# Optimization experiments

Measured on AMD Instinct MI355X. Metric: run time of the kernel, lower is better.

The kernel has to match this reference:

```python
import jax, jax.numpy as jnp
import numpy as np

N_NODES = 65536
N_GRAPHS = 1024
NODES_PER_G = 64
N_EDGES = 1048576
IN_FEATS = 512
HIDDEN = 1024
H4 = 256
EMB = 512
EPS = 1e-5
SLOPE = 0.01


def setup_inputs() -> dict:
    key = jax.random.key(0)
    ks = jax.random.split(key, 10)
    # within-graph random edges: edge e belongs to graph e // (E/B)
    epg = N_EDGES // N_GRAPHS
    eg = np.arange(N_EDGES) // epg
    rng = np.random.default_rng(0)
    src = rng.integers(0, NODES_PER_G, N_EDGES) + eg * NODES_PER_G
    dst = rng.integers(0, NODES_PER_G, N_EDGES) + eg * NODES_PER_G
    node_gid = np.arange(N_NODES) // NODES_PER_G
    return {
        "node_feats": jax.random.normal(ks[0], (N_NODES, IN_FEATS), jnp.float32),
        "edge_weights": jax.random.uniform(ks[1], (N_EDGES,), jnp.float32),
        "W1": jax.random.normal(ks[2], (IN_FEATS, HIDDEN), jnp.float32) * 0.05,
        "W2": jax.random.normal(ks[3], (HIDDEN, H4), jnp.float32) * 0.05,
        "W_emb": jax.random.normal(ks[4], (IN_FEATS + HIDDEN + H4, EMB), jnp.float32) * 0.02,
        "gn1_alpha": jnp.ones((HIDDEN,), jnp.float32),
        "gn1_gamma": jnp.ones((HIDDEN,), jnp.float32),
        "gn1_beta": jnp.zeros((HIDDEN,), jnp.float32),
        "gn2_alpha": jnp.ones((H4,), jnp.float32),
        "gn2_gamma": jnp.ones((H4,), jnp.float32),
        "gn2_beta": jnp.zeros((H4,), jnp.float32),
        "edge_src": jnp.asarray(src, jnp.int32),
        "edge_dst": jnp.asarray(dst, jnp.int32),
        "node_gid": jnp.asarray(node_gid, jnp.int32),
    }


def _seg_sum(x, ids, num):
    return jax.ops.segment_sum(x, ids, num_segments=num)


def _graph_conv(x, W, src, dst, ew):
    # DGL GraphConv, norm='both', bias=False, with edge_weight (u_mul_e)
    ones = jnp.ones((src.shape[0],), x.dtype)
    deg_out = jnp.clip(_seg_sum(ones, src, N_NODES), 1.0)
    deg_in = jnp.clip(_seg_sum(ones, dst, N_NODES), 1.0)
    h = (x * jax.lax.rsqrt(deg_out)[:, None]) @ W
    msg = h[src] * ew[:, None]
    agg = _seg_sum(msg, dst, N_NODES)
    return agg * jax.lax.rsqrt(deg_in)[:, None]


def _graph_norm(x, gid, counts, alpha, gamma, beta):
    # GraphNorm (Cai et al.): learnable mean-scale alpha, per-graph stats
    mean = _seg_sum(x, gid, N_GRAPHS) / counts[:, None]
    sub = x - alpha * mean[gid]
    var = _seg_sum(sub * sub, gid, N_GRAPHS) / counts[:, None]
    return gamma * sub * jax.lax.rsqrt(var[gid] + EPS) + beta


def _mean_nodes(x, gid, counts):
    return _seg_sum(x, gid, N_GRAPHS) / counts[:, None]


def _leaky(x):
    return jnp.where(x >= 0, x, SLOPE * x)


def reference(node_feats, edge_weights, W1, W2, W_emb,
              gn1_alpha, gn1_gamma, gn1_beta,
              gn2_alpha, gn2_gamma, gn2_beta,
              edge_src, edge_dst, node_gid):
    counts = jnp.clip(_seg_sum(jnp.ones((N_NODES,), node_feats.dtype), node_gid, N_GRAPHS), 1.0)
    r0 = _mean_nodes(node_feats, node_gid, counts)                 # [B, in]
    h1 = _graph_conv(node_feats, W1, edge_src, edge_dst, edge_weights)
    h1 = _leaky(_graph_norm(h1, node_gid, counts, gn1_alpha, gn1_gamma, gn1_beta))
    r1 = _mean_nodes(h1, node_gid, counts)                          # [B, hidden]
    h2 = _graph_conv(h1, W2, edge_src, edge_dst, edge_weights)
    h2 = _leaky(_graph_norm(h2, node_gid, counts, gn2_alpha, gn2_gamma, gn2_beta))
    r2 = _mean_nodes(h2, node_gid, counts)                          # [B, hidden/4]
    emb = jnp.concatenate([r0, r1, r2], axis=1) @ W_emb             # [B, EMB]
    # InstanceNorm1d on [B, E] input: per-row normalization, no affine
    mu = jnp.mean(emb, axis=1, keepdims=True)
    var = jnp.mean((emb - mu) ** 2, axis=1, keepdims=True)
    emb = (emb - mu) * jax.lax.rsqrt(var + EPS)
    return _leaky(emb)
```

## Files before the change

### kernel.cpp

```cpp
#include <hip/hip_runtime.h>
#include <hip/hip_bf16.h>
#include <stdint.h>

#define N_NODES   65536
#define N_GRAPHS  1024
#define N_EDGES   1048576
#define IN_FEATS  512
#define HIDDEN    1024
#define H4        256
#define EMB_DIM   512
#define RDIM      1792
#define EPS_F     1e-5f
#define SLOPE_F   0.01f

typedef __bf16 bf16;
typedef __bf16 bf16x8 __attribute__((ext_vector_type(8)));
typedef float  floatx4 __attribute__((ext_vector_type(4)));

#define GLDS16(gp, lp) __builtin_amdgcn_global_load_lds( \
    (const __attribute__((address_space(1))) void*)(gp), \
    (__attribute__((address_space(3))) void*)(lp), 16, 0, 0)

__global__ __launch_bounds__(256) void k_graph_build(
    const int* __restrict__ src, const int* __restrict__ dst,
    const float* __restrict__ ew,
    bf16* __restrict__ adjb, float* __restrict__ scl_o)
{
    __shared__ float sAdj[4096];
    __shared__ float sDegO[64], sDegI[64];
    int g = blockIdx.x, tid = threadIdx.x;
    for (int i = tid; i < 4096; i += 256) sAdj[i] = 0.f;
    if (tid < 64) { sDegO[tid] = 0.f; sDegI[tid] = 0.f; }
    __syncthreads();
    int e0 = g * 1024;
    #pragma unroll
    for (int i = 0; i < 4; ++i) {
        int e = e0 + i * 256 + tid;
        int s = src[e] & 63, d = dst[e] & 63;
        atomicAdd(&sAdj[(d << 6) | s], ew[e]);
        atomicAdd(&sDegO[s], 1.f);
        atomicAdd(&sDegI[d], 1.f);
    }
    __syncthreads();
    if (tid < 64) scl_o[g * 64 + tid] = rsqrtf(fmaxf(sDegO[tid], 1.f));
    bf16* ag = adjb + ((size_t)g << 12);
    for (int i = tid; i < 4096; i += 256) {
        float si = rsqrtf(fmaxf(sDegI[i >> 6], 1.f));
        ag[i] = (bf16)(sAdj[i] * si);
    }
}

__global__ __launch_bounds__(256) void k_transpose(
    const float* __restrict__ W, bf16* __restrict__ WT, int K, int logN)
{
    int idx = blockIdx.x * 256 + threadIdx.x;
    if (idx >= (K << logN)) return;
    int n = idx & ((1 << logN) - 1);
    int k = idx >> logN;
    WT[(size_t)n * K + k] = (bf16)W[idx];
}

__global__ __launch_bounds__(256) void k_prep_agg1(
    const float* __restrict__ x, const float* __restrict__ so,
    const bf16* __restrict__ adjb,
    bf16* __restrict__ axs1, bf16* __restrict__ Rb)
{
    __shared__ __align__(16) bf16 sOut[64 * 264];
    __shared__ float sSo[64];
    int g = blockIdx.x >> 1, half = blockIdx.x & 1;
    int tid = threadIdx.x, lane = tid & 63, wave = tid >> 6, q = lane >> 4;
    if (tid < 64) sSo[tid] = so[g * 64 + tid];
    const float* xg = x + (size_t)g * 64 * IN_FEATS + half * 256;
    const bf16* ag = adjb + ((size_t)g << 12);

    bf16x8 af[4][2];
    #pragma unroll
    for (int mt = 0; mt < 4; ++mt)
        #pragma unroll
        for (int kk = 0; kk < 2; ++kk)
            af[mt][kk] = *(const bf16x8*)&ag[(mt * 16 + (lane & 15)) * 64 + kk * 32 + q * 8];
    __syncthreads();
    float sov[2][8];
    #pragma unroll
    for (int kk = 0; kk < 2; ++kk)
        #pragma unroll
        for (int j = 0; j < 8; ++j) sov[kk][j] = sSo[kk * 32 + q * 8 + j];

    #pragma unroll
    for (int nt = 0; nt < 4; ++nt) {
        int cl = wave * 64 + nt * 16 + (lane & 15);
        floatx4 acc[4] = {};
        float r0 = 0.f;
        #pragma unroll
        for (int kk = 0; kk < 2; ++kk) {
            bf16x8 bfrag;
            #pragma unroll
            for (int j = 0; j < 8; ++j) {
                float v = xg[(size_t)(kk * 32 + q * 8 + j) * IN_FEATS + cl];
                r0 += v;
                bfrag[j] = (bf16)(v * sov[kk][j]);
            }
            #pragma unroll
            for (int mt = 0; mt < 4; ++mt)
                acc[mt] = __builtin_amdgcn_mfma_f32_16x16x32_bf16(af[mt][kk], bfrag, acc[mt], 0, 0, 0);
        }
        r0 += __shfl_xor(r0, 16);
        r0 += __shfl_xor(r0, 32);
        if (lane < 16) Rb[(size_t)g * RDIM + half * 256 + cl] = (bf16)(r0 * (1.f / 64.f));
        #pragma unroll
        for (int mt = 0; mt < 4; ++mt)
            #pragma unroll
            for (int i = 0; i < 4; ++i)
                sOut[(mt * 16 + q * 4 + i) * 264 + cl] = (bf16)acc[mt][i];
    }
    __syncthreads();
    #pragma unroll
    for (int it = 0; it < 8; ++it) {
        int idx = it * 256 + tid;
        int d = idx >> 5, c8 = idx & 31;
        *(bf16x8*)&axs1[(size_t)(g * 64 + d) * IN_FEATS + half * 256 + c8 * 8] =
            *(const bf16x8*)&sOut[d * 264 + c8 * 8];
    }
}

__device__ __forceinline__ void gemm_mainloop_db(
    const bf16* __restrict__ A, const bf16* __restrict__ BT, int K,
    int row0, int col0, int lane, int wave, int wm, int wn, int q,
    bf16* sm, floatx4 (&acc)[4][4])
{
    auto stage = [&](int k0, int buf) {
        #pragma unroll
        for (int i = 0; i < 4; ++i) {
            int u = (wave * 4 + i) * 64 + lane;
            int r = u >> 3, c = (u & 7) ^ (r & 7);
            GLDS16(A  + (size_t)(row0 + r) * K + (k0 + c * 8),
                   sm + buf * 16384 + (wave * 4 + i) * 512);
            GLDS16(BT + (size_t)(col0 + r) * K + (k0 + c * 8),
                   sm + buf * 16384 + 8192 + (wave * 4 + i) * 512);
        }
    };
    auto step = [&](int buf) {
        const bf16* sA = sm + buf * 16384;
        const bf16* sB = sA + 8192;
        #pragma unroll
        for (int kk = 0; kk < 2; ++kk) {
            bf16x8 afr[4], bfr[4];
            int cw = kk * 4 + q;
            #pragma unroll
            for (int mt = 0; mt < 4; ++mt) {
                int r = wm * 64 + mt * 16 + (lane & 15);
                afr[mt] = *(const bf16x8*)&sA[(r * 8 + (cw ^ (r & 7))) * 8];
            }
            #pragma unroll
            for (int nt = 0; nt < 4; ++nt) {
                int r = wn * 64 + nt * 16 + (lane & 15);
                bfr[nt] = *(const bf16x8*)&sB[(r * 8 + (cw ^ (r & 7))) * 8];
            }
            #pragma unroll
            for (int mt = 0; mt < 4; ++mt)
                #pragma unroll
                for (int nt = 0; nt < 4; ++nt)
                    acc[mt][nt] = __builtin_amdgcn_mfma_f32_16x16x32_bf16(
                        afr[mt], bfr[nt], acc[mt][nt], 0, 0, 0);
        }
    };
    stage(0, 0);
    asm volatile("s_waitcnt vmcnt(0)" ::: "memory");
    __syncthreads();
    int cur = 0;
    const int nsteps = K >> 6;
    #pragma unroll 1
    for (int t = 0; t < nsteps - 1; ++t) {
        stage((t + 1) << 6, cur ^ 1);
        step(cur);
        asm volatile("s_waitcnt vmcnt(0)" ::: "memory");
        __syncthreads();
        cur ^= 1;
    }
    step(cur);
}

__device__ __forceinline__ void swizzle_block(int cb, int& bx, int& by)
{
    int b = blockIdx.y * gridDim.x + blockIdx.x;
    int xcd = b & 7, t = b >> 3;
    bx = t % cb;
    by = (t / cb) * 8 + xcd;
}

__global__ __launch_bounds__(256) void k_gemm1_f(
    const bf16* __restrict__ A, const bf16* __restrict__ BT,
    const float* __restrict__ alpha, const float* __restrict__ gamma,
    const float* __restrict__ beta,
    const float* __restrict__ so,
    bf16* __restrict__ xs2, bf16* __restrict__ Rb)
{
    __shared__ __align__(16) bf16 sm[32768];
    __shared__ float sSo[128];
    const int tid = threadIdx.x;
    const int lane = tid & 63, wave = tid >> 6, q = lane >> 4;
    const int wm = wave & 1, wn = wave >> 1;
    int bx, by; swizzle_block(gridDim.x, bx, by);
    const int row0 = by * 128, col0 = bx * 128;

    if (tid < 128) sSo[tid] = so[row0 + tid];

    floatx4 acc[4][4] = {};
    gemm_mainloop_db(A, BT, IN_FEATS, row0, col0, lane, wave, wm, wn, q, sm, acc);
    __syncthreads();

    const int gw = by * 2 + wm;
    bf16* sOut = sm;
    #pragma unroll
    for (int nt = 0; nt < 4; ++nt) {
        int cl = wn * 64 + nt * 16 + (lane & 15);
        int colg = col0 + cl;
        float lsum = 0.f;
        #pragma unroll
        for (int mt = 0; mt < 4; ++mt)
            #pragma unroll
            for (int i = 0; i < 4; ++i) lsum += acc[mt][nt][i];
        lsum += __shfl_xor(lsum, 16);
        lsum += __shfl_xor(lsum, 32);
        float am = alpha[colg] * (lsum * (1.f / 64.f));
        float gm = gamma[colg], bt = beta[colg];
        float sub[4][4], qv = 0.f;
        #pragma unroll
        for (int mt = 0; mt < 4; ++mt)
            #pragma unroll
            for (int i = 0; i < 4; ++i) {
                float d = acc[mt][nt][i] - am;
                sub[mt][i] = d; qv += d * d;
            }
        qv += __shfl_xor(qv, 16);
        qv += __shfl_xor(qv, 32);
        float rs = rsqrtf(qv * (1.f / 64.f) + EPS_F);
        float rsum = 0.f;
        #pragma unroll
        for (int mt = 0; mt < 4; ++mt)
            #pragma unroll
            for (int i = 0; i < 4; ++i) {
                float o = gm * sub[mt][i] * rs + bt;
                o = (o >= 0.f) ? o : SLOPE_F * o;
                rsum += o;
                int r = wm * 64 + mt * 16 + q * 4 + i;
                sOut[r * 136 + cl] = (bf16)(o * sSo[r]);
            }
        rsum += __shfl_xor(rsum, 16);
        rsum += __shfl_xor(rsum, 32);
        if (lane < 16)
            Rb[(size_t)gw * RDIM + 512 + colg] = (bf16)(rsum * (1.f / 64.f));
    }
    __syncthreads();
    #pragma unroll
    for (int it = 0; it < 8; ++it) {
        int idx = it * 256 + tid;
        int r = idx >> 4, c8 = idx & 15;
        *(bf16x8*)&xs2[(size_t)(row0 + r) * HIDDEN + col0 + c8 * 8] =
            *(const bf16x8*)&sOut[r * 136 + c8 * 8];
    }
}

__global__ __launch_bounds__(256) void k_gemm2_f(
    const bf16* __restrict__ A, const bf16* __restrict__ BT,
    const bf16* __restrict__ adjb,
    const float* __restrict__ alpha, const float* __restrict__ gamma,
    const float* __restrict__ beta,
    bf16* __restrict__ Rb)
{
    __shared__ __align__(16) bf16 sm[32768];
    const int tid = threadIdx.x;
    const int lane = tid & 63, wave = tid >> 6, q = lane >> 4;
    const int wm = wave & 1, wn = wave >> 1;
    int bx, by; swizzle_block(gridDim.x, bx, by);
    const int row0 = by * 128, col0 = bx * 128;

    floatx4 acc[4][4] = {};
    gemm_mainloop_db(A, BT, HIDDEN, row0, col0, lane, wave, wm, wn, q, sm, acc);
    __syncthreads();

    bf16* sT = sm;
    #pragma unroll
    for (int nt = 0; nt < 4; ++nt) {
        int cl = wn * 64 + nt * 16 + (lane & 15);
        #pragma unroll
        for (int mt = 0; mt < 4; ++mt)
            #pragma unroll
            for (int i = 0; i < 4; ++i)
                sT[cl * 136 + wm * 64 + mt * 16 + q * 4 + i] = (bf16)acc[mt][nt][i];
    }
    asm volatile("s_waitcnt lgkmcnt(0)" ::: "memory");

    const int gw = by * 2 + wm;
    const bf16* ag = adjb + ((size_t)gw << 12);
    floatx4 a2[4][4] = {};
    #pragma unroll
    for (int kk = 0; kk < 2; ++kk) {
        bf16x8 afr[4], bfr[4];
        #pragma unroll
        for (int mt = 0; mt < 4; ++mt)
            afr[mt] = *(const bf16x8*)&ag[(mt * 16 + (lane & 15)) * 64 + kk * 32 + q * 8];
        #pragma unroll
        for (int nt = 0; nt < 4; ++nt)
            bfr[nt] = *(const bf16x8*)&sT[(wn * 64 + nt * 16 + (lane & 15)) * 136 + wm * 64 + kk * 32 + q * 8];
        #pragma unroll
        for (int mt = 0; mt < 4; ++mt)
            #pragma unroll
            for (int nt = 0; nt < 4; ++nt)
                a2[mt][nt] = __builtin_amdgcn_mfma_f32_16x16x32_bf16(afr[mt], bfr[nt], a2[mt][nt], 0, 0, 0);
    }

    #pragma unroll
    for (int nt = 0; nt < 4; ++nt) {
        int colg = col0 + wn * 64 + nt * 16 + (lane & 15);
        float lsum = 0.f;
        #pragma unroll
        for (int mt = 0; mt < 4; ++mt)
            #pragma unroll
            for (int i = 0; i < 4; ++i) lsum += a2[mt][nt][i];
        lsum += __shfl_xor(lsum, 16);
        lsum += __shfl_xor(lsum, 32);
        float am = alpha[colg] * (lsum * (1.f / 64.f));
        float gm = gamma[colg], bt = beta[colg];
        float sub[4][4], qv = 0.f;
        #pragma unroll
        for (int mt = 0; mt < 4; ++mt)
            #pragma unroll
            for (int i = 0; i < 4; ++i) {
                float d = a2[mt][nt][i] - am;
                sub[mt][i] = d; qv += d * d;
            }
        qv += __shfl_xor(qv, 16);
        qv += __shfl_xor(qv, 32);
        float rs = rsqrtf(qv * (1.f / 64.f) + EPS_F);
        float rsum = 0.f;
        #pragma unroll
        for (int mt = 0; mt < 4; ++mt)
            #pragma unroll
            for (int i = 0; i < 4; ++i) {
                float o = gm * sub[mt][i] * rs + bt;
                rsum += (o >= 0.f) ? o : SLOPE_F * o;
            }
        rsum += __shfl_xor(rsum, 16);
        rsum += __shfl_xor(rsum, 32);
        if (lane < 16)
            Rb[(size_t)gw * RDIM + 1536 + colg] = (bf16)(rsum * (1.f / 64.f));
    }
}

__global__ __launch_bounds__(256) void k_gemm_ro(
    const bf16* __restrict__ A, const bf16* __restrict__ BT,
    float* __restrict__ Cout)
{
    __shared__ __align__(16) bf16 sm[32768];
    const int tid = threadIdx.x;
    const int lane = tid & 63, wave = tid >> 6, q = lane >> 4;
    const int wm = wave & 1, wn = wave >> 1;
    int bx, by; swizzle_block(gridDim.x, bx, by);
    const int row0 = by * 128, col0 = bx * 128;

    floatx4 acc[4][4] = {};
    gemm_mainloop_db(A, BT, RDIM, row0, col0, lane, wave, wm, wn, q, sm, acc);

    #pragma unroll
    for (int mt = 0; mt < 4; ++mt)
        #pragma unroll
        for (int nt = 0; nt < 4; ++nt) {
            int col = col0 + wn * 64 + nt * 16 + (lane & 15);
            #pragma unroll
            for (int i = 0; i < 4; ++i) {
                int row = row0 + wm * 64 + mt * 16 + q * 4 + i;
                Cout[(size_t)row * EMB_DIM + col] = acc[mt][nt][i];
            }
        }
}

__global__ __launch_bounds__(256) void k_instnorm(
    const float* __restrict__ emb, float* __restrict__ out)
{
    int row = blockIdx.x, tid = threadIdx.x;
    int lane = tid & 63, wave = tid >> 6;
    __shared__ float sS[4], sQ[4];
    float v0 = emb[(size_t)row * EMB_DIM + tid];
    float v1 = emb[(size_t)row * EMB_DIM + 256 + tid];
    float s = v0 + v1, q = v0 * v0 + v1 * v1;
    #pragma unroll
    for (int off = 32; off; off >>= 1) {
        s += __shfl_down(s, off);
        q += __shfl_down(q, off);
    }
    if (lane == 0) { sS[wave] = s; sQ[wave] = q; }
    __syncthreads();
    float S = sS[0] + sS[1] + sS[2] + sS[3];
    float Q = sQ[0] + sQ[1] + sQ[2] + sQ[3];
    float mu = S * (1.f / 512.f);
    float var = Q * (1.f / 512.f) - mu * mu;
    float rs = rsqrtf(var + EPS_F);
    float o0 = (v0 - mu) * rs; o0 = (o0 >= 0.f) ? o0 : SLOPE_F * o0;
    float o1 = (v1 - mu) * rs; o1 = (o1 >= 0.f) ? o1 : SLOPE_F * o1;
    out[(size_t)row * EMB_DIM + tid]       = o0;
    out[(size_t)row * EMB_DIM + 256 + tid] = o1;
}

extern "C" void kernel_launch(void* const* d_in, const int* in_sizes, int n_in,
                              void* d_out, int out_size, void* d_ws, size_t ws_size,
                              hipStream_t stream) {
    const float* x    = (const float*)d_in[0];
    const float* ew   = (const float*)d_in[1];
    const float* W1   = (const float*)d_in[2];
    const float* W2   = (const float*)d_in[3];
    const float* Wemb = (const float*)d_in[4];
    const float* a1   = (const float*)d_in[5];
    const float* g1   = (const float*)d_in[6];
    const float* b1   = (const float*)d_in[7];
    const float* a2   = (const float*)d_in[8];
    const float* g2   = (const float*)d_in[9];
    const float* b2   = (const float*)d_in[10];
    const int* esrc   = (const int*)d_in[11];
    const int* edst   = (const int*)d_in[12];
    float* out = (float*)d_out;

    char* ws = (char*)d_ws;
    const size_t MB = 1024ull * 1024ull;
    bf16*  adjb   = (bf16*)(ws);
    float* scl_o  = (float*)(ws + 8 * MB);
    bf16*  Rb     = (bf16*)(ws + 9 * MB);
    bf16*  W1T    = (bf16*)(ws + 13 * MB);
    bf16*  W2T    = (bf16*)(ws + 14 * MB);
    bf16*  WembT  = (bf16*)(ws + 15 * MB);
    float* emb    = (float*)(ws + 17 * MB);
    bf16*  axs1   = (bf16*)(ws + 20 * MB);
    bf16*  xs2    = (bf16*)(ws + 84 * MB);

    k_graph_build<<<N_GRAPHS, 256, 0, stream>>>(esrc, edst, ew, adjb, scl_o);
    k_transpose<<<2048, 256, 0, stream>>>(W1, W1T, 512, 10);
    k_transpose<<<1024, 256, 0, stream>>>(W2, W2T, 1024, 8);
    k_transpose<<<3584, 256, 0, stream>>>(Wemb, WembT, 1792, 9);

    k_prep_agg1<<<N_GRAPHS * 2, 256, 0, stream>>>(x, scl_o, adjb, axs1, Rb);

    k_gemm1_f<<<dim3(HIDDEN / 128, N_NODES / 128), 256, 0, stream>>>(
        axs1, W1T, a1, g1, b1, scl_o, xs2, Rb);
    k_gemm2_f<<<dim3(H4 / 128, N_NODES / 128), 256, 0, stream>>>(
        xs2, W2T, adjb, a2, g2, b2, Rb);
    k_gemm_ro<<<dim3(EMB_DIM / 128, N_GRAPHS / 128), 256, 0, stream>>>(
        Rb, WembT, emb);
    k_instnorm<<<N_GRAPHS, 256, 0, stream>>>(emb, out);

    (void)in_sizes; (void)n_in; (void)out_size; (void)ws_size;
}
```

Measured before the change: 470.6 us.

## Fuse layer-1 GEMM, GraphNorm and layer-2 GEMM into one kernel

Merges the two GEMM kernels into a single 512-thread kernel in which each block owns 128 node rows. It loops over the eight 128-column tiles of the hidden layer, applies GraphNorm and LeakyReLU in registers, and feeds the result from shared memory straight into the second GEMM with W2. This removes the 128 MB round trip of the hidden activation xs2 through global memory and one launch. In exchange the grid drops to 512 blocks, W1 and W2 are reloaded by every block, LDS use is large (about 100 KB), and the loop over column tiles is serialized with extra barriers.

```diff
diff --git a/kernel.cpp b/kernel.cpp
--- a/kernel.cpp
+++ b/kernel.cpp
@@ -120,6 +120,228 @@
         int d = idx >> 5, c8 = idx & 31;
         *(bf16x8*)&axs1[(size_t)(g * 64 + d) * IN_FEATS + half * 256 + c8 * 8] =
             *(const bf16x8*)&sOut[d * 264 + c8 * 8];
+    }
+}
+
+__global__ __launch_bounds__(512) void k_gemm12(
+    const bf16* __restrict__ A, const bf16* __restrict__ BT1,
+    const bf16* __restrict__ BT2, const bf16* __restrict__ adjb,
+    const float* __restrict__ al1, const float* __restrict__ ga1, const float* __restrict__ be1,
+    const float* __restrict__ al2, const float* __restrict__ ga2, const float* __restrict__ be2,
+    const float* __restrict__ so, bf16* __restrict__ Rb)
+{
+    __shared__ __align__(16) bf16 sm[50176];
+    __shared__ float sSo[128];
+    const int tid = threadIdx.x;
+    const int lane = tid & 63, wave = tid >> 6, q = lane >> 4;
+    const int wm = wave >> 2, wn = wave & 3;
+    const int by = blockIdx.x;
+    const int row0 = by * 128;
+    const int gw = by * 2 + wm;
+    if (tid < 128) sSo[tid] = so[row0 + tid];
+
+    floatx4 acc2[4][4] = {};
+    bf16* sX = sm + 32768;
+
+    #pragma unroll 1
+    for (int ct = 0; ct < 8; ++ct) {
+        floatx4 acc1[4][2] = {};
+
+        auto stage_ab = [&](int k0, int buf) {
+            #pragma unroll
+            for (int ro = 0; ro < 2; ++ro) {
+                int u = ro * 4096 + wave * 512 + lane * 8;
+                int r = u >> 6, c = ((u >> 3) & 7) ^ (r & 7);
+                GLDS16(A   + (size_t)(row0 + r) * IN_FEATS + k0 + c * 8,
+                       sm + buf * 16384 + ro * 4096 + wave * 512);
+                GLDS16(BT1 + (size_t)(ct * 128 + r) * IN_FEATS + k0 + c * 8,
+                       sm + buf * 16384 + 8192 + ro * 4096 + wave * 512);
+            }
+        };
+        auto stage_w2 = [&](int h) {
+            #pragma unroll
+            for (int ro = 0; ro < 4; ++ro) {
+                int u = ro * 4096 + wave * 512 + lane * 8;
+                int r = u >> 6, c = ((u >> 3) & 7) ^ (r & 7);
+                GLDS16(BT2 + (size_t)r * HIDDEN + ct * 128 + h * 64 + c * 8,
+                       sm + h * 16384 + ro * 4096 + wave * 512);
+            }
+        };
+        auto mfma_step = [&](int buf) {
+            const bf16* sA = sm + buf * 16384;
+            const bf16* sB = sA + 8192;
+            #pragma unroll
+            for (int kk = 0; kk < 2; ++kk) {
+                bf16x8 afr[4], bfr[2];
+                int cw = kk * 4 + q;
+                #pragma unroll
+                for (int mt = 0; mt < 4; ++mt) {
+                    int r = wm * 64 + mt * 16 + (lane & 15);
+                    afr[mt] = *(const bf16x8*)&sA[(r * 8 + (cw ^ (r & 7))) * 8];
+                }
+                #pragma unroll
+                for (int nt = 0; nt < 2; ++nt) {
+                    int r = wn * 32 + nt * 16 + (lane & 15);
+                    bfr[nt] = *(const bf16x8*)&sB[(r * 8 + (cw ^ (r & 7))) * 8];
+                }
+                #pragma unroll
+                for (int mt = 0; mt < 4; ++mt)
+                    #pragma unroll
+                    for (int nt = 0; nt < 2; ++nt)
+                        acc1[mt][nt] = __builtin_amdgcn_mfma_f32_16x16x32_bf16(
+                            afr[mt], bfr[nt], acc1[mt][nt], 0, 0, 0);
+            }
+        };
+
+        stage_ab(0, 0);
+        asm volatile("s_waitcnt vmcnt(0)" ::: "memory");
+        __syncthreads();
+
+        int cur = 0;
+        #pragma unroll 1
+        for (int t = 0; t < 7; ++t) {
+            stage_ab((t + 1) * 64, cur ^ 1);
+            mfma_step(cur);
+            asm volatile("s_waitcnt vmcnt(0)" ::: "memory");
+            __syncthreads();
+            cur ^= 1;
+        }
+        stage_w2(0);
+        mfma_step(1);
+        __syncthreads();
+        stage_w2(1);
+
+        #pragma unroll
+        for (int nt = 0; nt < 2; ++nt) {
+            int cl = wn * 32 + nt * 16 + (lane & 15);
+            int colg = ct * 128 + cl;
+            float lsum = 0.f;
+            #pragma unroll
+            for (int mt = 0; mt < 4; ++mt)
+                #pragma unroll
+                for (int i = 0; i < 4; ++i) lsum += acc1[mt][nt][i];
+            lsum += __shfl_xor(lsum, 16);
+            lsum += __shfl_xor(lsum, 32);
+            float am = al1[colg] * (lsum * (1.f / 64.f));
+            float gm = ga1[colg], bt = be1[colg];
+            float sub[4][4], qv = 0.f;
+            #pragma unroll
+            for (int mt = 0; mt < 4; ++mt)
+                #pragma unroll
+                for (int i = 0; i < 4; ++i) {
+                    float d = acc1[mt][nt][i] - am;
+                    sub[mt][i] = d; qv += d * d;
+                }
+            qv += __shfl_xor(qv, 16);
+            qv += __shfl_xor(qv, 32);
+            float rs = rsqrtf(qv * (1.f / 64.f) + EPS_F);
+            float rsum = 0.f;
+            #pragma unroll
+            for (int mt = 0; mt < 4; ++mt)
+                #pragma unroll
+                for (int i = 0; i < 4; ++i) {
+                    float o = gm * sub[mt][i] * rs + bt;
+                    o = (o >= 0.f) ? o : SLOPE_F * o;
+                    rsum += o;
+                    int r = wm * 64 + mt * 16 + q * 4 + i;
+                    sX[r * 136 + cl] = (bf16)(o * sSo[r]);
+                }
+            rsum += __shfl_xor(rsum, 16);
+            rsum += __shfl_xor(rsum, 32);
+            if (lane < 16)
+                Rb[(size_t)gw * RDIM + 512 + colg] = (bf16)(rsum * (1.f / 64.f));
+        }
+        asm volatile("s_waitcnt vmcnt(0)" ::: "memory");
+        __syncthreads();
+
+        #pragma unroll
+        for (int kk2 = 0; kk2 < 4; ++kk2) {
+            const bf16* sW = sm + (kk2 >> 1) * 16384;
+            int cw = (kk2 & 1) * 4 + q;
+            bf16x8 afr[4], bfr[4];
+            #pragma unroll
+            for (int mt = 0; mt < 4; ++mt)
+                afr[mt] = *(const bf16x8*)&sX[(wm * 64 + mt * 16 + (lane & 15)) * 136 + kk2 * 32 + q * 8];
+            #pragma unroll
+            for (int nt = 0; nt < 4; ++nt) {
+                int r = wn * 64 + nt * 16 + (lane & 15);
+                bfr[nt] = *(const bf16x8*)&sW[(r * 8 + (cw ^ (r & 7))) * 8];
+            }
+            #pragma unroll
+            for (int mt = 0; mt < 4; ++mt)
+                #pragma unroll
+                for (int nt = 0; nt < 4; ++nt)
+                    acc2[mt][nt] = __builtin_amdgcn_mfma_f32_16x16x32_bf16(
+                        afr[mt], bfr[nt], acc2[mt][nt], 0, 0, 0);
+        }
+        __syncthreads();
+    }
+
+    bf16* sT = sm;
+    #pragma unroll
+    for (int nt = 0; nt < 4; ++nt) {
+        int cl = wn * 64 + nt * 16 + (lane & 15);
+        #pragma unroll
+        for (int mt = 0; mt < 4; ++mt)
+            #pragma unroll
+            for (int i = 0; i < 4; ++i)
+                sT[cl * 136 + wm * 64 + mt * 16 + q * 4 + i] = (bf16)acc2[mt][nt][i];
+    }
+    asm volatile("s_waitcnt lgkmcnt(0)" ::: "memory");
+
+    const bf16* ag = adjb + ((size_t)gw << 12);
+    floatx4 hh[4][4] = {};
+    #pragma unroll
+    for (int kk = 0; kk < 2; ++kk) {
+        bf16x8 afr[4], bfr[4];
+        #pragma unroll
+        for (int mt = 0; mt < 4; ++mt)
+            afr[mt] = *(const bf16x8*)&ag[(mt * 16 + (lane & 15)) * 64 + kk * 32 + q * 8];
+        #pragma unroll
+        for (int nt = 0; nt < 4; ++nt)
+            bfr[nt] = *(const bf16x8*)&sT[(wn * 64 + nt * 16 + (lane & 15)) * 136 + wm * 64 + kk * 32 + q * 8];
+        #pragma unroll
+        for (int mt = 0; mt < 4; ++mt)
+            #pragma unroll
+            for (int nt = 0; nt < 4; ++nt)
+                hh[mt][nt] = __builtin_amdgcn_mfma_f32_16x16x32_bf16(afr[mt], bfr[nt], hh[mt][nt], 0, 0, 0);
+    }
+
+    #pragma unroll
+    for (int nt = 0; nt < 4; ++nt) {
+        int colg = wn * 64 + nt * 16 + (lane & 15);
+        float lsum = 0.f;
+        #pragma unroll
+        for (int mt = 0; mt < 4; ++mt)
+            #pragma unroll
+            for (int i = 0; i < 4; ++i) lsum += hh[mt][nt][i];
+        lsum += __shfl_xor(lsum, 16);
+        lsum += __shfl_xor(lsum, 32);
+        float am = al2[colg] * (lsum * (1.f / 64.f));
+        float gm = ga2[colg], bt = be2[colg];
+        float sub[4][4], qv = 0.f;
+        #pragma unroll
+        for (int mt = 0; mt < 4; ++mt)
+            #pragma unroll
+            for (int i = 0; i < 4; ++i) {
+                float d = hh[mt][nt][i] - am;
+                sub[mt][i] = d; qv += d * d;
+            }
+        qv += __shfl_xor(qv, 16);
+        qv += __shfl_xor(qv, 32);
+        float rs = rsqrtf(qv * (1.f / 64.f) + EPS_F);
+        float rsum = 0.f;
+        #pragma unroll
+        for (int mt = 0; mt < 4; ++mt)
+            #pragma unroll
+            for (int i = 0; i < 4; ++i) {
+                float o = gm * sub[mt][i] * rs + bt;
+                rsum += (o >= 0.f) ? o : SLOPE_F * o;
+            }
+        rsum += __shfl_xor(rsum, 16);
+        rsum += __shfl_xor(rsum, 32);
+        if (lane < 16)
+            Rb[(size_t)gw * RDIM + 1536 + colg] = (bf16)(rsum * (1.f / 64.f));
     }
 }
 
@@ -186,166 +408,6 @@
     int xcd = b & 7, t = b >> 3;
     bx = t % cb;
     by = (t / cb) * 8 + xcd;
-}
-
-__global__ __launch_bounds__(256) void k_gemm1_f(
-    const bf16* __restrict__ A, const bf16* __restrict__ BT,
-    const float* __restrict__ alpha, const float* __restrict__ gamma,
-    const float* __restrict__ beta,
-    const float* __restrict__ so,
-    bf16* __restrict__ xs2, bf16* __restrict__ Rb)
-{
-    __shared__ __align__(16) bf16 sm[32768];
-    __shared__ float sSo[128];
-    const int tid = threadIdx.x;
-    const int lane = tid & 63, wave = tid >> 6, q = lane >> 4;
-    const int wm = wave & 1, wn = wave >> 1;
-    int bx, by; swizzle_block(gridDim.x, bx, by);
-    const int row0 = by * 128, col0 = bx * 128;
-
-    if (tid < 128) sSo[tid] = so[row0 + tid];
-
-    floatx4 acc[4][4] = {};
-    gemm_mainloop_db(A, BT, IN_FEATS, row0, col0, lane, wave, wm, wn, q, sm, acc);
-    __syncthreads();
-
-    const int gw = by * 2 + wm;
-    bf16* sOut = sm;
-    #pragma unroll
-    for (int nt = 0; nt < 4; ++nt) {
-        int cl = wn * 64 + nt * 16 + (lane & 15);
-        int colg = col0 + cl;
-        float lsum = 0.f;
-        #pragma unroll
-        for (int mt = 0; mt < 4; ++mt)
-            #pragma unroll
-            for (int i = 0; i < 4; ++i) lsum += acc[mt][nt][i];
-        lsum += __shfl_xor(lsum, 16);
-        lsum += __shfl_xor(lsum, 32);
-        float am = alpha[colg] * (lsum * (1.f / 64.f));
-        float gm = gamma[colg], bt = beta[colg];
-        float sub[4][4], qv = 0.f;
-        #pragma unroll
-        for (int mt = 0; mt < 4; ++mt)
-            #pragma unroll
-            for (int i = 0; i < 4; ++i) {
-                float d = acc[mt][nt][i] - am;
-                sub[mt][i] = d; qv += d * d;
-            }
-        qv += __shfl_xor(qv, 16);
-        qv += __shfl_xor(qv, 32);
-        float rs = rsqrtf(qv * (1.f / 64.f) + EPS_F);
-        float rsum = 0.f;
-        #pragma unroll
-        for (int mt = 0; mt < 4; ++mt)
-            #pragma unroll
-            for (int i = 0; i < 4; ++i) {
-                float o = gm * sub[mt][i] * rs + bt;
-                o = (o >= 0.f) ? o : SLOPE_F * o;
-                rsum += o;
-                int r = wm * 64 + mt * 16 + q * 4 + i;
-                sOut[r * 136 + cl] = (bf16)(o * sSo[r]);
-            }
-        rsum += __shfl_xor(rsum, 16);
-        rsum += __shfl_xor(rsum, 32);
-        if (lane < 16)
-            Rb[(size_t)gw * RDIM + 512 + colg] = (bf16)(rsum * (1.f / 64.f));
-    }
-    __syncthreads();
-    #pragma unroll
-    for (int it = 0; it < 8; ++it) {
-        int idx = it * 256 + tid;
-        int r = idx >> 4, c8 = idx & 15;
-        *(bf16x8*)&xs2[(size_t)(row0 + r) * HIDDEN + col0 + c8 * 8] =
-            *(const bf16x8*)&sOut[r * 136 + c8 * 8];
-    }
-}
-
-__global__ __launch_bounds__(256) void k_gemm2_f(
-    const bf16* __restrict__ A, const bf16* __restrict__ BT,
-    const bf16* __restrict__ adjb,
-    const float* __restrict__ alpha, const float* __restrict__ gamma,
-    const float* __restrict__ beta,
-    bf16* __restrict__ Rb)
-{
-    __shared__ __align__(16) bf16 sm[32768];
-    const int tid = threadIdx.x;
-    const int lane = tid & 63, wave = tid >> 6, q = lane >> 4;
-    const int wm = wave & 1, wn = wave >> 1;
-    int bx, by; swizzle_block(gridDim.x, bx, by);
-    const int row0 = by * 128, col0 = bx * 128;
-
-    floatx4 acc[4][4] = {};
-    gemm_mainloop_db(A, BT, HIDDEN, row0, col0, lane, wave, wm, wn, q, sm, acc);
-    __syncthreads();
-
-    bf16* sT = sm;
-    #pragma unroll
-    for (int nt = 0; nt < 4; ++nt) {
-        int cl = wn * 64 + nt * 16 + (lane & 15);
-        #pragma unroll
-        for (int mt = 0; mt < 4; ++mt)
-            #pragma unroll
-            for (int i = 0; i < 4; ++i)
-                sT[cl * 136 + wm * 64 + mt * 16 + q * 4 + i] = (bf16)acc[mt][nt][i];
-    }
-    asm volatile("s_waitcnt lgkmcnt(0)" ::: "memory");
-
-    const int gw = by * 2 + wm;
-    const bf16* ag = adjb + ((size_t)gw << 12);
-    floatx4 a2[4][4] = {};
-    #pragma unroll
-    for (int kk = 0; kk < 2; ++kk) {
-        bf16x8 afr[4], bfr[4];
-        #pragma unroll
-        for (int mt = 0; mt < 4; ++mt)
-            afr[mt] = *(const bf16x8*)&ag[(mt * 16 + (lane & 15)) * 64 + kk * 32 + q * 8];
-        #pragma unroll
-        for (int nt = 0; nt < 4; ++nt)
-            bfr[nt] = *(const bf16x8*)&sT[(wn * 64 + nt * 16 + (lane & 15)) * 136 + wm * 64 + kk * 32 + q * 8];
-        #pragma unroll
-        for (int mt = 0; mt < 4; ++mt)
-            #pragma unroll
-            for (int nt = 0; nt < 4; ++nt)
-                a2[mt][nt] = __builtin_amdgcn_mfma_f32_16x16x32_bf16(afr[mt], bfr[nt], a2[mt][nt], 0, 0, 0);
-    }
-
-    #pragma unroll
-    for (int nt = 0; nt < 4; ++nt) {
-        int colg = col0 + wn * 64 + nt * 16 + (lane & 15);
-        float lsum = 0.f;
-        #pragma unroll
-        for (int mt = 0; mt < 4; ++mt)
-            #pragma unroll
-            for (int i = 0; i < 4; ++i) lsum += a2[mt][nt][i];
-        lsum += __shfl_xor(lsum, 16);
-        lsum += __shfl_xor(lsum, 32);
-        float am = alpha[colg] * (lsum * (1.f / 64.f));
-        float gm = gamma[colg], bt = beta[colg];
-        float sub[4][4], qv = 0.f;
-        #pragma unroll
-        for (int mt = 0; mt < 4; ++mt)
-            #pragma unroll
-            for (int i = 0; i < 4; ++i) {
-                float d = a2[mt][nt][i] - am;
-                sub[mt][i] = d; qv += d * d;
-            }
-        qv += __shfl_xor(qv, 16);
-        qv += __shfl_xor(qv, 32);
-        float rs = rsqrtf(qv * (1.f / 64.f) + EPS_F);
-        float rsum = 0.f;
-        #pragma unroll
-        for (int mt = 0; mt < 4; ++mt)
-            #pragma unroll
-            for (int i = 0; i < 4; ++i) {
-                float o = gm * sub[mt][i] * rs + bt;
-                rsum += (o >= 0.f) ? o : SLOPE_F * o;
-            }
-        rsum += __shfl_xor(rsum, 16);
-        rsum += __shfl_xor(rsum, 32);
-        if (lane < 16)
-            Rb[(size_t)gw * RDIM + 1536 + colg] = (bf16)(rsum * (1.f / 64.f));
-    }
 }
 
 __global__ __launch_bounds__(256) void k_gemm_ro(
@@ -430,7 +492,6 @@
     bf16*  WembT  = (bf16*)(ws + 15 * MB);
     float* emb    = (float*)(ws + 17 * MB);
     bf16*  axs1   = (bf16*)(ws + 20 * MB);
-    bf16*  xs2    = (bf16*)(ws + 84 * MB);
 
     k_graph_build<<<N_GRAPHS, 256, 0, stream>>>(esrc, edst, ew, adjb, scl_o);
     k_transpose<<<2048, 256, 0, stream>>>(W1, W1T, 512, 10);
@@ -439,10 +500,9 @@
 
     k_prep_agg1<<<N_GRAPHS * 2, 256, 0, stream>>>(x, scl_o, adjb, axs1, Rb);
 
-    k_gemm1_f<<<dim3(HIDDEN / 128, N_NODES / 128), 256, 0, stream>>>(
-        axs1, W1T, a1, g1, b1, scl_o, xs2, Rb);
-    k_gemm2_f<<<dim3(H4 / 128, N_NODES / 128), 256, 0, stream>>>(
-        xs2, W2T, adjb, a2, g2, b2, Rb);
+    k_gemm12<<<N_NODES / 128, 512, 0, stream>>>(
+        axs1, W1T, W2T, adjb, a1, g1, b1, a2, g2, b2, scl_o, Rb);
+
     k_gemm_ro<<<dim3(EMB_DIM / 128, N_GRAPHS / 128), 256, 0, stream>>>(
         Rb, WembT, emb);
     k_instnorm<<<N_GRAPHS, 256, 0, stream>>>(emb, out);
```

Measured after the change: 474.5 us. No clear change (+0.8%).
